# Kernel tuning notes

Hardware: AMD Instinct MI355X
Metric: run time of the kernel (lower is better)

## Reference

```python
import jax, jax.numpy as jnp
import numpy as np

B, T, C = 4, 4096, 1024
HEAD_SIZE = 64
HEAD_OUT = 64


def setup_inputs() -> dict:
    key = jax.random.key(0)
    kx, kk, kq, kv = jax.random.split(key, 4)
    x = jax.random.normal(kx, (B, T, C), dtype=jnp.float32)
    # nn.Linear(in, out, bias=False): weight [out, in]; y = x @ W.T
    Wk = jax.random.normal(kk, (HEAD_SIZE, C), dtype=jnp.float32) * (C ** -0.5)
    Wq = jax.random.normal(kq, (HEAD_SIZE, C), dtype=jnp.float32) * (C ** -0.5)
    Wv = jax.random.normal(kv, (HEAD_OUT, C), dtype=jnp.float32) * (C ** -0.5)
    return {"x": x, "Wk": Wk, "Wq": Wq, "Wv": Wv}


def reference(x, Wk, Wq, Wv):
    Tlen = x.shape[1]
    k = jnp.einsum('btc,hc->bth', x, Wk)  # [B,T,Hs]
    q = jnp.einsum('btc,hc->bth', x, Wq)  # [B,T,Hs]
    v = jnp.einsum('btc,oc->bto', x, Wv)  # [B,T,Ho]
    scale = HEAD_SIZE ** -0.5
    scores = jnp.einsum('bih,bjh->bij', q, k) * scale  # [B,T,T]
    # torch.tril(ones, diagonal=1): allowed where j <= i+1 (note: one superdiagonal kept)
    i = jnp.arange(Tlen)[:, None]
    j = jnp.arange(Tlen)[None, :]
    allowed = j <= i + 1
    masked = jnp.where(allowed, scores, -jnp.inf)
    # NOTE: original scales AGAIN inside softmax (double scaling, faithful)
    weights = jax.nn.softmax(masked * scale, axis=-1)
    return jnp.einsum('bij,bjo->bio', weights, v)  # [B,T,Ho]
```

## Files before the change

### kernel.cpp

```cpp
#include <hip/hip_runtime.h>

#define BB 4
#define TT 4096
#define CC 1024
#define HH 64
#define AW 8

#define OS 35
#define LSB (64 * OS)
#define SHROW 2276

typedef unsigned short us;
typedef us v8u __attribute__((ext_vector_type(8)));
typedef us v4u __attribute__((ext_vector_type(4)));
typedef __bf16 v8bf __attribute__((ext_vector_type(8)));
typedef float v4f __attribute__((ext_vector_type(4)));

__device__ __forceinline__ us f2bf(float f) {
  return __builtin_bit_cast(us, (__bf16)f);
}
__device__ __forceinline__ v8bf ldb(const us* p) {
  return __builtin_bit_cast(v8bf, *(const v8u*)p);
}

__global__ __launch_bounds__(256) void convertw_kernel(const float* __restrict__ Wk,
                                                       const float* __restrict__ Wq,
                                                       const float* __restrict__ Wv,
                                                       us* __restrict__ wpack) {
  const int g = blockIdx.x * 256 + threadIdx.x;
  const int t = g >> 13;
  const int rem = g & 8191;
  const int oc = rem >> 11;
  const int kc = (rem >> 6) & 31;
  const int lane = rem & 63;
  const float* W = (t == 0) ? Wq : ((t == 1) ? Wk : Wv);
  const int h  = oc * 16 + (lane & 15);
  const int d0 = kc * 32 + (lane >> 4) * 8;
  const float4* src = (const float4*)(W + h * CC + d0);
  const float4 f0 = src[0], f1 = src[1];
  v8u o;
  o[0]=f2bf(f0.x); o[1]=f2bf(f0.y); o[2]=f2bf(f0.z); o[3]=f2bf(f0.w);
  o[4]=f2bf(f1.x); o[5]=f2bf(f1.y); o[6]=f2bf(f1.z); o[7]=f2bf(f1.w);
  *(v8u*)(wpack + (size_t)g * 8) = o;
}


__global__ __launch_bounds__(768, 6) void proj_kernel(
    const float* __restrict__ x, const us* __restrict__ wpack,
    us* __restrict__ qpack, us* __restrict__ kpack, us* __restrict__ vpack)
{
  __shared__ __align__(16) us xlds[32][1048];

  const int tid  = threadIdx.x;
  const int lane = tid & 63, w = tid >> 6;
  const int i16 = lane & 15, quad = lane >> 4;
  const int t = w >> 2, oc = w & 3;
  const int rows0 = blockIdx.x * 32;

  const float4* xg4 = (const float4*)(x + (size_t)rows0 * CC);
  for (int i = tid; i < 8192; i += 768) {
    const float4 f = xg4[i];
    v4u o; o[0]=f2bf(f.x); o[1]=f2bf(f.y); o[2]=f2bf(f.z); o[3]=f2bf(f.w);
    *(v4u*)&xlds[i >> 8][(i & 255) * 4] = o;
  }
  __syncthreads();

  const us* wp = wpack + (size_t)w * 16384 + lane * 8;
  v4f zero = {0.f, 0.f, 0.f, 0.f};
  v4f acc[2] = {zero, zero};

  v8bf wf = ldb(wp);
  #pragma unroll 4
  for (int kc = 0; kc < 32; kc++) {
    const v8bf wnxt = ldb(wp + ((kc + 1) & 31) * 512);
    #pragma unroll
    for (int rg = 0; rg < 2; rg++) {
      const v8bf a = ldb(&xlds[rg * 16 + i16][kc * 32 + quad * 8]);
      acc[rg] = __builtin_amdgcn_mfma_f32_16x16x32_bf16(a, wf, acc[rg], 0, 0, 0);
    }
    wf = wnxt;
  }

  const float COEF = 0.015625f * 1.4426950408889634f;
  const int b    = rows0 >> 12;
  const int tile = (rows0 & (TT - 1)) >> 5;

  if (t < 2) {
    us* dst = t ? kpack : qpack;
    const float c = t ? 1.0f : COEF;
    const int h = oc * 16 + i16;
    #pragma unroll
    for (int rg = 0; rg < 2; rg++) {
      #pragma unroll
      for (int r = 0; r < 4; r++) {
        const int tr = quad * 4 + r;
        const int lane2 = tr + 16 * ((h >> 3) & 3);
        const size_t idx = ((((size_t)(b * 128 + tile) * 2 + rg) * 2 + (h >> 5)) * 64 + lane2) * 8 + (h & 7);
        dst[idx] = f2bf(acc[rg][r] * c);
      }
    }
  } else {
    #pragma unroll
    for (int rg = 0; rg < 2; rg++) {
      const int lane3 = i16 + 16 * (rg * 2 + (quad >> 1));
      v4u pk;
      #pragma unroll
      for (int r = 0; r < 4; r++) pk[r] = f2bf(acc[rg][r]);
      *(v4u*)&vpack[(((size_t)(b * 128 + tile) * 4 + oc) * 64 + lane3) * 8 + (quad & 1) * 4] = pk;
    }
  }
}

__global__ __launch_bounds__(512, 4) void attn_kernel(
    const us* __restrict__ qpack, const us* __restrict__ kpack,
    const us* __restrict__ vpack, float* __restrict__ out)
{
  __shared__ float shbuf[AW][SHROW];

  const int tid  = threadIdx.x;
  const int lane = tid & 63, warp = tid >> 6;
  const int i16 = lane & 15, quad = lane >> 4;

  const int p = blockIdx.x & 255, s = blockIdx.x >> 8;
  const int b  = p & 3;
  const int q0 = p >> 2;
  const int qb = s ? (127 - q0) : q0;
  const int i0 = qb << 5;
  const int nt = min(qb + 2, 128);

  us* Pw = (us*)shbuf[warp];
  const float NEGINF = -__builtin_inff();

  v8bf qf[2][2];
  #pragma unroll
  for (int ih = 0; ih < 2; ih++)
    #pragma unroll
    for (int g = 0; g < 2; g++)
      qf[ih][g] = ldb(qpack + ((((size_t)(b * 128 + qb) * 2 + ih) * 2 + g) * 64 + lane) * 8);

  v4f zero = {0.f, 0.f, 0.f, 0.f};
  v4f oacc[2][4];
  #pragma unroll
  for (int ih = 0; ih < 2; ih++)
    #pragma unroll
    for (int oc = 0; oc < 4; oc++) oacc[ih][oc] = zero;
  float lsum[2] = {0.f, 0.f};

  auto loadK = [&](int t, v8bf kf[2][2]) {
    #pragma unroll
    for (int f = 0; f < 2; f++)
      #pragma unroll
      for (int g = 0; g < 2; g++)
        kf[f][g] = ldb(kpack + ((((size_t)(b * 128 + t) * 2 + f) * 2 + g) * 64 + lane) * 8);
  };
  auto loadV = [&](int t, v8bf vf[4]) {
    #pragma unroll
    for (int oc = 0; oc < 4; oc++)
      vf[oc] = ldb(vpack + (((size_t)(b * 128 + t) * 4 + oc) * 64 + lane) * 8);
  };
  auto qk_exp_store = [&](int t, const v8bf kf[2][2], int buf) {
    v4f sacc[2][2];
    #pragma unroll
    for (int ih = 0; ih < 2; ih++)
      #pragma unroll
      for (int f = 0; f < 2; f++) {
        v4f sv = zero;
        sv = __builtin_amdgcn_mfma_f32_16x16x32_bf16(kf[f][0], qf[ih][0], sv, 0, 0, 0);
        sv = __builtin_amdgcn_mfma_f32_16x16x32_bf16(kf[f][1], qf[ih][1], sv, 0, 0, 0);
        sacc[ih][f] = sv;
      }
    const int j0 = t * 32;
    const bool needMask = (t >= qb);
    #pragma unroll
    for (int ih = 0; ih < 2; ih++) {
      float ps[8];
      #pragma unroll
      for (int f = 0; f < 2; f++)
        #pragma unroll
        for (int r = 0; r < 4; r++) {
          float sv = fminf(sacc[ih][f][r], 80.f);
          if (needMask) {
            const int j = j0 + f * 16 + quad * 4 + r;
            const int i = i0 + ih * 16 + i16;
            sv = (j <= i + 1) ? sv : NEGINF;
          }
          ps[f * 4 + r] = exp2f(sv);
        }
      {
        const float s0 = ps[0] + ps[1], s1 = ps[2] + ps[3];
        const float s2 = ps[4] + ps[5], s3 = ps[6] + ps[7];
        lsum[ih] += (s0 + s1) + (s2 + s3);
      }
      #pragma unroll
      for (int f = 0; f < 2; f++) {
        v4u pk;
        #pragma unroll
        for (int r = 0; r < 4; r++) pk[r] = f2bf(ps[f * 4 + r]);
        *(v4u*)&Pw[buf * 1280 + ih * 640 + i16 * 40 + f * 16 + quad * 4] = pk;
      }
    }
  };
  auto pv = [&](int buf, const v8bf vf[4]) {
    #pragma unroll
    for (int ih = 0; ih < 2; ih++) {
      v8bf pf = __builtin_bit_cast(v8bf, *(const v8u*)&Pw[buf * 1280 + ih * 640 + i16 * 40 + quad * 8]);
      #pragma unroll
      for (int oc = 0; oc < 4; oc++)
        oacc[ih][oc] = __builtin_amdgcn_mfma_f32_16x16x32_bf16(vf[oc], pf, oacc[ih][oc], 0, 0, 0);
    }
  };

  int t = warp, buf = 0;
  if (t < nt) {
    v8bf kcur[2][2], knxt[2][2], vprev[4];
    loadK(t, kcur); loadV(t, vprev);
    if (t + AW < nt) loadK(t + AW, knxt);
    qk_exp_store(t, kcur, 0);
    #pragma unroll 2
    for (t += AW; t < nt; t += AW) {
      pv(buf, vprev);
      loadV(t, vprev);
      #pragma unroll
      for (int f = 0; f < 2; f++)
        #pragma unroll
        for (int g = 0; g < 2; g++) kcur[f][g] = knxt[f][g];
      if (t + AW < nt) loadK(t + AW, knxt);
      qk_exp_store(t, kcur, buf ^ 1);
      buf ^= 1;
    }
    pv(buf, vprev);
  }

  #pragma unroll
  for (int ih = 0; ih < 2; ih++) {
    lsum[ih] += __shfl_xor(lsum[ih], 16, 64);
    lsum[ih] += __shfl_xor(lsum[ih], 32, 64);
    #pragma unroll
    for (int oc = 0; oc < 4; oc++)
      #pragma unroll
      for (int r = 0; r < 4; r++)
        shbuf[warp][(oc * 16 + quad * 4 + r) * OS + ih * 16 + i16] = oacc[ih][oc][r];
  }
  if (lane < 16) {
    shbuf[warp][LSB + lane]      = lsum[0];
    shbuf[warp][LSB + 16 + lane] = lsum[1];
  }
  __syncthreads();

  const int o  = tid & 63;
  const int iw = tid >> 6;
  #pragma unroll
  for (int rr = 0; rr < 4; rr++) {
    const int i = iw + rr * 8;
    float L = 0.f, O = 0.f;
    #pragma unroll
    for (int w = 0; w < AW; w++) {
      L += shbuf[w][LSB + i];
      O += shbuf[w][o * OS + i];
    }
    out[(size_t)(b * TT + i0 + i) * HH + o] = O / L;
  }
}

extern "C" void kernel_launch(void* const* d_in, const int* in_sizes, int n_in,
                              void* d_out, int out_size, void* d_ws, size_t ws_size,
                              hipStream_t stream) {
  const size_t NWP = 3 * 4 * 32 * 64 * 8;
  const size_t NP  = (size_t)BB * TT * HH;

  us* wpack = (us*)d_ws;
  us* qpack = wpack + NWP;
  us* kpack = qpack + NP;
  us* vpack = kpack + NP;
  float* out = (float*)d_out;

  convertw_kernel<<<96, 256, 0, stream>>>(
      (const float*)d_in[1], (const float*)d_in[2], (const float*)d_in[3], wpack);
  proj_kernel<<<BB * TT / 32, 768, 0, stream>>>(
      (const float*)d_in[0], wpack, qpack, kpack, vpack);
  attn_kernel<<<512, 512, 0, stream>>>(qpack, kpack, vpack, out);
}
```

Before: 129.1 us.

## Split projection x staging into two halves and raise MFMA wave priority in attention

The projection kernel now stages x in two 16-row halves. It loads the second half into registers while the MFMA loop runs on the first half, so the global load overlaps compute. The weight fragments are reloaded from global in each half's loop instead of being prefetched one step ahead, which doubles weight traffic. Separately, the attention kernel wraps its QK and PV MFMA blocks in s_setprio(1)/s_setprio(0) so waves issuing matrix ops get scheduling priority over waves doing exp and stores. The register-held prefetch (6 float4 per thread) adds register pressure at 768 threads per block.

After: 132.4 us. 1.03x slower.

```diff
diff --git a/kernel.cpp b/kernel.cpp
--- a/kernel.cpp
+++ b/kernel.cpp
@@ -49,7 +49,7 @@
     const float* __restrict__ x, const us* __restrict__ wpack,
     us* __restrict__ qpack, us* __restrict__ kpack, us* __restrict__ vpack)
 {
-  __shared__ __align__(16) us xlds[32][1048];
+  __shared__ __align__(16) us xlds[2][16][1048];
 
   const int tid  = threadIdx.x;
   const int lane = tid & 63, w = tid >> 6;
@@ -58,27 +58,51 @@
   const int rows0 = blockIdx.x * 32;
 
   const float4* xg4 = (const float4*)(x + (size_t)rows0 * CC);
-  for (int i = tid; i < 8192; i += 768) {
-    const float4 f = xg4[i];
-    v4u o; o[0]=f2bf(f.x); o[1]=f2bf(f.y); o[2]=f2bf(f.z); o[3]=f2bf(f.w);
-    *(v4u*)&xlds[i >> 8][(i & 255) * 4] = o;
+
+  #pragma unroll
+  for (int j = 0; j < 6; j++) {
+    const int i = tid + j * 768;
+    if (i < 4096) {
+      const float4 f = xg4[i];
+      v4u o; o[0]=f2bf(f.x); o[1]=f2bf(f.y); o[2]=f2bf(f.z); o[3]=f2bf(f.w);
+      *(v4u*)&xlds[0][i >> 8][(i & 255) * 4] = o;
+    }
   }
   __syncthreads();
+
+  float4 fB[6];
+  #pragma unroll
+  for (int j = 0; j < 6; j++) {
+    const int i = tid + j * 768;
+    if (i < 4096) fB[j] = xg4[4096 + i];
+  }
 
   const us* wp = wpack + (size_t)w * 16384 + lane * 8;
   v4f zero = {0.f, 0.f, 0.f, 0.f};
   v4f acc[2] = {zero, zero};
 
-  v8bf wf = ldb(wp);
   #pragma unroll 4
   for (int kc = 0; kc < 32; kc++) {
-    const v8bf wnxt = ldb(wp + ((kc + 1) & 31) * 512);
-    #pragma unroll
-    for (int rg = 0; rg < 2; rg++) {
-      const v8bf a = ldb(&xlds[rg * 16 + i16][kc * 32 + quad * 8]);
-      acc[rg] = __builtin_amdgcn_mfma_f32_16x16x32_bf16(a, wf, acc[rg], 0, 0, 0);
-    }
-    wf = wnxt;
+    const v8bf wf = ldb(wp + kc * 512);
+    const v8bf a = ldb(&xlds[0][i16][kc * 32 + quad * 8]);
+    acc[0] = __builtin_amdgcn_mfma_f32_16x16x32_bf16(a, wf, acc[0], 0, 0, 0);
+  }
+
+  #pragma unroll
+  for (int j = 0; j < 6; j++) {
+    const int i = tid + j * 768;
+    if (i < 4096) {
+      v4u o; o[0]=f2bf(fB[j].x); o[1]=f2bf(fB[j].y); o[2]=f2bf(fB[j].z); o[3]=f2bf(fB[j].w);
+      *(v4u*)&xlds[1][i >> 8][(i & 255) * 4] = o;
+    }
+  }
+  __syncthreads();
+
+  #pragma unroll 4
+  for (int kc = 0; kc < 32; kc++) {
+    const v8bf wf = ldb(wp + kc * 512);
+    const v8bf a = ldb(&xlds[1][i16][kc * 32 + quad * 8]);
+    acc[1] = __builtin_amdgcn_mfma_f32_16x16x32_bf16(a, wf, acc[1], 0, 0, 0);
   }
 
   const float COEF = 0.015625f * 1.4426950408889634f;
@@ -160,6 +184,7 @@
   };
   auto qk_exp_store = [&](int t, const v8bf kf[2][2], int buf) {
     v4f sacc[2][2];
+    __builtin_amdgcn_s_setprio(1);
     #pragma unroll
     for (int ih = 0; ih < 2; ih++)
       #pragma unroll
@@ -169,6 +194,7 @@
         sv = __builtin_amdgcn_mfma_f32_16x16x32_bf16(kf[f][1], qf[ih][1], sv, 0, 0, 0);
         sacc[ih][f] = sv;
       }
+    __builtin_amdgcn_s_setprio(0);
     const int j0 = t * 32;
     const bool needMask = (t >= qb);
     #pragma unroll
@@ -201,6 +227,7 @@
     }
   };
   auto pv = [&](int buf, const v8bf vf[4]) {
+    __builtin_amdgcn_s_setprio(1);
     #pragma unroll
     for (int ih = 0; ih < 2; ih++) {
       v8bf pf = __builtin_bit_cast(v8bf, *(const v8u*)&Pw[buf * 1280 + ih * 640 + i16 * 40 + quad * 8]);
@@ -208,6 +235,7 @@
       for (int oc = 0; oc < 4; oc++)
         oacc[ih][oc] = __builtin_amdgcn_mfma_f32_16x16x32_bf16(vf[oc], pf, oacc[ih][oc], 0, 0, 0);
     }
+    __builtin_amdgcn_s_setprio(0);
   };
 
   int t = warp, buf = 0;
```
